# Kernel tuning notes

Measured on AMD Instinct MI355X. Metric: run time of the kernel, lower is better.

Reference implementation:

```python
import jax, jax.numpy as jnp
import numpy as np

B, G, GS = 1024, 2000, 25   # batch, num gene groups, group size
H1, H2, C = 1024, 512, 10
EPS = 1e-5


def _xavier(key, shape, fan_in, fan_out):
    lim = np.sqrt(6.0 / (fan_in + fan_out))
    return jax.random.uniform(key, shape, jnp.float32, -lim, lim)


def setup_inputs() -> dict:
    key = jax.random.key(0)
    ks = jax.random.split(key, 8)
    x = jax.random.normal(ks[0], (B, G * GS), jnp.float32)
    # per-group Linear(GS, 1) weights stacked -> block-diagonal grouped GEMM
    gene_w = _xavier(ks[1], (G, GS), GS, 1)
    gene_b = jnp.zeros((G,), jnp.float32)
    W1 = _xavier(ks[2], (G, H1), G, H1)
    b1 = jnp.zeros((H1,), jnp.float32)
    W2 = _xavier(ks[3], (H1, H2), H1, H2)
    b2 = jnp.zeros((H2,), jnp.float32)
    Wout = _xavier(ks[4], (H2, C), H2, C)
    bout = jnp.zeros((C,), jnp.float32)
    Wres = _xavier(ks[5], (G, C), G, C)
    bres = jnp.zeros((C,), jnp.float32)
    gamma1 = jnp.ones((H1,), jnp.float32); beta1 = jnp.zeros((H1,), jnp.float32)
    gamma2 = jnp.ones((H2,), jnp.float32); beta2 = jnp.zeros((H2,), jnp.float32)
    return dict(x=x, gene_w=gene_w, gene_b=gene_b, W1=W1, b1=b1,
                gamma1=gamma1, beta1=beta1, W2=W2, b2=b2,
                gamma2=gamma2, beta2=beta2, Wout=Wout, bout=bout,
                Wres=Wres, bres=bres)


def _batch_norm(h, gamma, beta):
    # training-mode BatchNorm1d: biased batch statistics over axis 0
    mu = jnp.mean(h, axis=0)
    var = jnp.mean(jnp.square(h - mu), axis=0)
    return gamma * (h - mu) * jax.lax.rsqrt(var + EPS) + beta


def reference(x, gene_w, gene_b, W1, b1, gamma1, beta1, W2, b2,
              gamma2, beta2, Wout, bout, Wres, bres):
    # fused replacement for the per-group Linear(GS,1)+ReLU loop + cat
    xg = x.reshape(B, G, GS)
    g = jax.nn.relu(jnp.einsum('bgk,gk->bg', xg, gene_w) + gene_b)  # [B, G]
    h1 = jax.nn.relu(_batch_norm(g @ W1 + b1, gamma1, beta1))       # [B, H1]
    h2 = jax.nn.relu(_batch_norm(h1 @ W2 + b2, gamma2, beta2))      # [B, H2]
    x_main = h2 @ Wout + bout                                       # [B, C]
    x_res = g @ Wres + bres                                         # [B, C]
    return jax.nn.softmax(x_main + x_res, axis=1)
```

## Files before the change

### kernel.cpp

```cpp
#include <hip/hip_runtime.h>
#include <math.h>

#define NB   1024
#define NG   2000
#define NGS  25
#define KP   2048
#define NH1  1024
#define NH2  512
#define NC   10
#define EPSV 1e-5f
#define GPB  200

typedef __attribute__((ext_vector_type(8))) __bf16 bf16x8;
typedef __attribute__((ext_vector_type(4))) float f32x4;
typedef __attribute__((ext_vector_type(8))) unsigned short u16x8;
typedef __attribute__((ext_vector_type(4))) unsigned short u16x4;

__device__ __forceinline__ unsigned short f2bf(float f) {
  union { float f; unsigned u; } v; v.f = f;
  return (unsigned short)((v.u + 0x7fffu + ((v.u >> 16) & 1u)) >> 16);
}
__device__ __forceinline__ float bf2f(unsigned short b) {
  union { unsigned u; float f; } v; v.u = ((unsigned)b) << 16;
  return v.f;
}

__global__ __launch_bounds__(256) void prep_kernel(
    const float* __restrict__ x, const float* __restrict__ gw,
    const float* __restrict__ gb, unsigned short* __restrict__ g_bf,
    const float* __restrict__ W1, unsigned short* __restrict__ W1bT,
    const float* __restrict__ W2, unsigned short* __restrict__ W2bT,
    float* __restrict__ stats) {
  __shared__ char smem[GPB * NGS * 4];
  int t = threadIdx.x;

  if (blockIdx.y < 10) {
    float* xs = (float*)smem;
    int b = blockIdx.x;
    int blk = blockIdx.y;
    const float4* src = (const float4*)(x + (size_t)b * (NG * NGS) + blk * (GPB * NGS));
    float4* dst = (float4*)xs;
    for (int i = t; i < (GPB * NGS) / 4; i += 256) dst[i] = src[i];
    __syncthreads();
    if (t < GPB) {
      int gi = blk * GPB + t;
      const float* wp = gw + gi * NGS;
      const float* xp = xs + t * NGS;
      float acc = 0.f;
#pragma unroll
      for (int k = 0; k < NGS; ++k) acc = fmaf(xp[k], wp[k], acc);
      acc += gb[gi];
      g_bf[(size_t)b * KP + gi] = f2bf(fmaxf(acc, 0.f));
    } else if (blk == 9 && t < GPB + (KP - NG)) {
      g_bf[(size_t)b * KP + NG + (t - GPB)] = 0;
    }
    return;
  }

  int bx = blockIdx.x;
  if (bx == 640) {
    for (int i = t; i < 3072; i += 256) stats[i] = 0.f;
    return;
  }
  const float* src; unsigned short* dst; int K, N, Kpad, k0, n0;
  if (bx < 512)      { src = W1; dst = W1bT; K = NG;  N = NH1; Kpad = KP;
                       k0 = (bx & 31) * 64; n0 = (bx >> 5) * 64; }
  else if (bx < 640) { int xi = bx - 512;
                       src = W2; dst = W2bT; K = NH1; N = NH2; Kpad = NH1;
                       k0 = (xi & 15) * 64; n0 = (xi >> 4) * 64; }
  else return;

  unsigned short (*ts)[72] = (unsigned short (*)[72])smem;
  int c4 = (t & 15) * 4;
  int r  = t >> 4;
  for (int rr = r; rr < 64; rr += 16) {
    int k = k0 + rr;
    float4 v = make_float4(0.f, 0.f, 0.f, 0.f);
    if (k < K) v = *(const float4*)&src[(size_t)k * N + n0 + c4];
    ts[rr][c4 + 0] = f2bf(v.x); ts[rr][c4 + 1] = f2bf(v.y);
    ts[rr][c4 + 2] = f2bf(v.z); ts[rr][c4 + 3] = f2bf(v.w);
  }
  __syncthreads();
  int rr8 = (t & 7) * 8;
  int cc  = t >> 3;
  for (int c = cc; c < 64; c += 32) {
    u16x8 val;
#pragma unroll
    for (int i = 0; i < 8; ++i) val[i] = ts[rr8 + i][c];
    *(u16x8*)&dst[(size_t)(n0 + c) * Kpad + k0 + rr8] = val;
  }
}

__global__ __launch_bounds__(256) void gemm1_kernel(
    const unsigned short* __restrict__ A,
    const unsigned short* __restrict__ Bt,
    float* __restrict__ C, float* __restrict__ sum, float* __restrict__ sq,
    int M, int N, int Kp) {
  __shared__ unsigned short As[32][72];
  __shared__ unsigned short Bs[64][72];
  int t = threadIdx.x;
  int m0 = blockIdx.y * 32, n0 = blockIdx.x * 64;
  int wave = t >> 6, lane = t & 63;
  int wm = (wave >> 1) * 16, wn = (wave & 1) * 32;
  int fm = lane & 15, fk = (lane >> 4) * 8;
  int srow = t >> 3, skc = (t & 7) * 8;

  f32x4 acc[2];
  acc[0] = (f32x4){0.f, 0.f, 0.f, 0.f};
  acc[1] = (f32x4){0.f, 0.f, 0.f, 0.f};

  const unsigned short* Ap = A + (size_t)(m0 + srow) * Kp + skc;
  const unsigned short* Bp = Bt + (size_t)(n0 + srow) * Kp + skc;
  size_t rstep = 32 * (size_t)Kp;

  u16x8 pa0 = *(const u16x8*)(Ap);
  u16x8 pb0 = *(const u16x8*)(Bp);
  u16x8 pb1 = *(const u16x8*)(Bp + rstep);

  for (int k0 = 0; k0 < Kp; k0 += 64) {
    *(u16x8*)&As[srow][skc]      = pa0;
    *(u16x8*)&Bs[srow][skc]      = pb0;
    *(u16x8*)&Bs[srow + 32][skc] = pb1;
    __syncthreads();
    if (k0 + 64 < Kp) {
      pa0 = *(const u16x8*)(Ap + k0 + 64);
      pb0 = *(const u16x8*)(Bp + k0 + 64);
      pb1 = *(const u16x8*)(Bp + k0 + 64 + rstep);
    }
#pragma unroll
    for (int s = 0; s < 2; ++s) {
      bf16x8 af = *(const bf16x8*)&As[wm + fm][s * 32 + fk];
      bf16x8 b0 = *(const bf16x8*)&Bs[wn + fm][s * 32 + fk];
      bf16x8 b1 = *(const bf16x8*)&Bs[wn + 16 + fm][s * 32 + fk];
      acc[0] = __builtin_amdgcn_mfma_f32_16x16x32_bf16(af, b0, acc[0], 0, 0, 0);
      acc[1] = __builtin_amdgcn_mfma_f32_16x16x32_bf16(af, b1, acc[1], 0, 0, 0);
    }
    __syncthreads();
  }

  int crow = (lane >> 4) * 4, ccol = lane & 15;
#pragma unroll
  for (int j = 0; j < 2; ++j) {
    float s = 0.f, ss = 0.f;
#pragma unroll
    for (int r = 0; r < 4; ++r) {
      float v = acc[j][r];
      int m = m0 + wm + crow + r;
      int n = n0 + wn + j * 16 + ccol;
      C[(size_t)m * N + n] = v;
      s += v;
      ss = fmaf(v, v, ss);
    }
    s  += __shfl_down(s, 32, 64);  s  += __shfl_down(s, 16, 64);
    ss += __shfl_down(ss, 32, 64); ss += __shfl_down(ss, 16, 64);
    if (lane < 16) {
      atomicAdd(&sum[n0 + wn + j * 16 + lane], s);
      atomicAdd(&sq[n0 + wn + j * 16 + lane], ss);
    }
  }
}

__global__ __launch_bounds__(256) void gemm2_kernel(
    const float* __restrict__ A,
    const unsigned short* __restrict__ Bt,
    float* __restrict__ C, const float* __restrict__ sum1,
    const float* __restrict__ sq1, const float* __restrict__ gam1,
    const float* __restrict__ bet1, float* __restrict__ sum2,
    float* __restrict__ sq2, int M, int N, int Kp) {
  __shared__ unsigned short As[32][72];
  __shared__ unsigned short Bs[32][72];
  int t = threadIdx.x;
  int m0 = blockIdx.y * 32, n0 = blockIdx.x * 32;
  int wave = t >> 6, lane = t & 63;
  int wm = (wave >> 1) * 16, wn = (wave & 1) * 16;
  int fm = lane & 15, fk = (lane >> 4) * 8;
  int srow = t >> 3, skc = (t & 7) * 8;

  f32x4 acc = (f32x4){0.f, 0.f, 0.f, 0.f};

  const float* Ap = A + (size_t)(m0 + srow) * Kp + skc;
  const unsigned short* Bp = Bt + (size_t)(n0 + srow) * Kp + skc;

  f32x4 pa0 = *(const f32x4*)(Ap);
  f32x4 pa1 = *(const f32x4*)(Ap + 4);
  u16x8 pb0 = *(const u16x8*)(Bp);

  for (int k0 = 0; k0 < Kp; k0 += 64) {
    float sc[8], sh[8];
#pragma unroll
    for (int i = 0; i < 8; ++i) {
      int k = k0 + skc + i;
      float mu  = sum1[k] * (1.f / NB);
      float var = sq1[k] * (1.f / NB) - mu * mu;
      float rs  = rsqrtf(var + EPSV);
      sc[i] = gam1[k] * rs;
      sh[i] = fmaf(-mu, sc[i], bet1[k]);
    }
    u16x8 a0;
#pragma unroll
    for (int i = 0; i < 4; ++i) {
      a0[i]     = f2bf(fmaxf(fmaf(pa0[i], sc[i],     sh[i]),     0.f));
      a0[i + 4] = f2bf(fmaxf(fmaf(pa1[i], sc[i + 4], sh[i + 4]), 0.f));
    }
    *(u16x8*)&As[srow][skc] = a0;
    *(u16x8*)&Bs[srow][skc] = pb0;
    __syncthreads();
    if (k0 + 64 < Kp) {
      pa0 = *(const f32x4*)(Ap + k0 + 64);
      pa1 = *(const f32x4*)(Ap + k0 + 64 + 4);
      pb0 = *(const u16x8*)(Bp + k0 + 64);
    }
#pragma unroll
    for (int s = 0; s < 2; ++s) {
      bf16x8 af = *(const bf16x8*)&As[wm + fm][s * 32 + fk];
      bf16x8 bf = *(const bf16x8*)&Bs[wn + fm][s * 32 + fk];
      acc = __builtin_amdgcn_mfma_f32_16x16x32_bf16(af, bf, acc, 0, 0, 0);
    }
    __syncthreads();
  }

  int crow = (lane >> 4) * 4, ccol = lane & 15;
  float s = 0.f, ss = 0.f;
#pragma unroll
  for (int r = 0; r < 4; ++r) {
    float v = acc[r];
    int m = m0 + wm + crow + r;
    int n = n0 + wn + ccol;
    C[(size_t)m * N + n] = v;
    s += v;
    ss = fmaf(v, v, ss);
  }
  s  += __shfl_down(s, 32, 64);  s  += __shfl_down(s, 16, 64);
  ss += __shfl_down(ss, 32, 64); ss += __shfl_down(ss, 16, 64);
  if (lane < 16) {
    atomicAdd(&sum2[n0 + wn + lane], s);
    atomicAdd(&sq2[n0 + wn + lane], ss);
  }
}

__global__ __launch_bounds__(256) void final_kernel(
    const float* __restrict__ t2, const float* __restrict__ sum2,
    const float* __restrict__ sq2, const float* __restrict__ gam2,
    const float* __restrict__ bet2, const unsigned short* __restrict__ g_bf,
    const float* __restrict__ Wout, const float* __restrict__ bout,
    const float* __restrict__ Wres, const float* __restrict__ bres,
    float* __restrict__ out) {
  int b = blockIdx.x;
  int t = threadIdx.x;
  float acc[NC] = {};

  if (t < NH2 / 4) {
    float4 tv = *(const float4*)&t2[(size_t)b * NH2 + t * 4];
    float raw[4] = {tv.x, tv.y, tv.z, tv.w};
    float hr[4];
#pragma unroll
    for (int i = 0; i < 4; ++i) {
      int c = t * 4 + i;
      float mu  = sum2[c] * (1.f / NB);
      float var = sq2[c] * (1.f / NB) - mu * mu;
      float rs  = rsqrtf(var + EPSV);
      float scv = gam2[c] * rs;
      hr[i] = fmaxf(fmaf(raw[i], scv, fmaf(-mu, scv, bet2[c])), 0.f);
    }
    const float4* wp = (const float4*)&Wout[t * 4 * NC];
    float w[40];
#pragma unroll
    for (int q = 0; q < 10; ++q) {
      float4 wv = wp[q];
      w[q * 4] = wv.x; w[q * 4 + 1] = wv.y; w[q * 4 + 2] = wv.z; w[q * 4 + 3] = wv.w;
    }
#pragma unroll
    for (int r = 0; r < 4; ++r)
#pragma unroll
      for (int c = 0; c < NC; ++c) acc[c] = fmaf(hr[r], w[r * NC + c], acc[c]);
  }

  for (int u = t; u < NG / 4; u += 256) {
    u16x4 gv = *(const u16x4*)&g_bf[(size_t)b * KP + u * 4];
    float gr[4] = {bf2f(gv[0]), bf2f(gv[1]), bf2f(gv[2]), bf2f(gv[3])};
    const float4* wp = (const float4*)&Wres[u * 4 * NC];
    float w[40];
#pragma unroll
    for (int q = 0; q < 10; ++q) {
      float4 wv = wp[q];
      w[q * 4] = wv.x; w[q * 4 + 1] = wv.y; w[q * 4 + 2] = wv.z; w[q * 4 + 3] = wv.w;
    }
#pragma unroll
    for (int r = 0; r < 4; ++r)
#pragma unroll
      for (int c = 0; c < NC; ++c) acc[c] = fmaf(gr[r], w[r * NC + c], acc[c]);
  }

  __shared__ float red[4][NC];
  __shared__ float logits[NC];
  int lane = t & 63, wave = t >> 6;
#pragma unroll
  for (int c = 0; c < NC; ++c) {
    float v = acc[c];
    for (int off = 32; off > 0; off >>= 1) v += __shfl_down(v, off, 64);
    if (lane == 0) red[wave][c] = v;
  }
  __syncthreads();
  if (t < NC)
    logits[t] = red[0][t] + red[1][t] + red[2][t] + red[3][t] + bout[t] + bres[t];
  __syncthreads();
  if (t == 0) {
    float mx = logits[0];
#pragma unroll
    for (int c = 1; c < NC; ++c) mx = fmaxf(mx, logits[c]);
    float e[NC], s = 0.f;
#pragma unroll
    for (int c = 0; c < NC; ++c) { e[c] = expf(logits[c] - mx); s += e[c]; }
    float inv = 1.f / s;
#pragma unroll
    for (int c = 0; c < NC; ++c) out[(size_t)b * NC + c] = e[c] * inv;
  }
}

extern "C" void kernel_launch(void* const* d_in, const int* in_sizes, int n_in,
                              void* d_out, int out_size, void* d_ws, size_t ws_size,
                              hipStream_t stream) {
  const float* x      = (const float*)d_in[0];
  const float* gw     = (const float*)d_in[1];
  const float* gb     = (const float*)d_in[2];
  const float* W1     = (const float*)d_in[3];
  const float* gamma1 = (const float*)d_in[5];
  const float* beta1  = (const float*)d_in[6];
  const float* W2     = (const float*)d_in[7];
  const float* gamma2 = (const float*)d_in[9];
  const float* beta2  = (const float*)d_in[10];
  const float* Wout   = (const float*)d_in[11];
  const float* bout   = (const float*)d_in[12];
  const float* Wres   = (const float*)d_in[13];
  const float* bres   = (const float*)d_in[14];
  float* out = (float*)d_out;

  char* p = (char*)d_ws;
  unsigned short* g_bf = (unsigned short*)p; p += (size_t)NB * KP * 2;
  unsigned short* W1bT = (unsigned short*)p; p += (size_t)NH1 * KP * 2;
  unsigned short* W2bT = (unsigned short*)p; p += (size_t)NH2 * NH1 * 2;
  float* t1 = (float*)p; p += (size_t)NB * NH1 * 4;
  float* t2 = (float*)p; p += (size_t)NB * NH2 * 4;
  float* stats = (float*)p;
  float* sum1 = stats, *sq1 = stats + 1024, *sum2 = stats + 2048, *sq2 = stats + 2560;

  prep_kernel<<<dim3(NB, 11), 256, 0, stream>>>(x, gw, gb, g_bf,
                                                W1, W1bT, W2, W2bT, stats);

  gemm1_kernel<<<dim3(NH1 / 64, NB / 32), 256, 0, stream>>>(
      g_bf, W1bT, t1, sum1, sq1, NB, NH1, KP);

  gemm2_kernel<<<dim3(NH2 / 32, NB / 32), 256, 0, stream>>>(
      t1, W2bT, t2, sum1, sq1, gamma1, beta1, sum2, sq2, NB, NH2, NH1);

  final_kernel<<<NB, 256, 0, stream>>>(t2, sum2, sq2, gamma2, beta2, g_bf,
                                       Wout, bout, Wres, bres, out);
}
```

Baseline: 366.2 us.

## Fuse GEMM1, GEMM2 and head into one cooperative kernel with grid syncs

Merges the three post-prep kernels into a single cooperative kernel of 512 blocks that uses grid-wide syncs in place of kernel boundaries. GEMM1 also switches to 32x32x16 MFMA with a 128-wide K tile, splitting K across wave pairs and reducing the two halves through shared memory. The aim is to cut launch gaps and raise MFMA efficiency in GEMM1. In exchange, the cooperative launch needs all 512 blocks resident at once, each stage is limited to 512 blocks, and the final softmax stage now handles two rows per block.

```diff
diff --git a/kernel.cpp b/kernel.cpp
--- a/kernel.cpp
+++ b/kernel.cpp
@@ -1,5 +1,8 @@
 #include <hip/hip_runtime.h>
+#include <hip/hip_cooperative_groups.h>
 #include <math.h>
+
+namespace cg = cooperative_groups;
 
 #define NB   1024
 #define NG   2000
@@ -11,10 +14,11 @@
 #define EPSV 1e-5f
 #define GPB  200
 
-typedef __attribute__((ext_vector_type(8))) __bf16 bf16x8;
-typedef __attribute__((ext_vector_type(4))) float f32x4;
-typedef __attribute__((ext_vector_type(8))) unsigned short u16x8;
-typedef __attribute__((ext_vector_type(4))) unsigned short u16x4;
+typedef __attribute__((ext_vector_type(8)))  __bf16 bf16x8;
+typedef __attribute__((ext_vector_type(4)))  float  f32x4;
+typedef __attribute__((ext_vector_type(16))) float  f32x16;
+typedef __attribute__((ext_vector_type(8)))  unsigned short u16x8;
+typedef __attribute__((ext_vector_type(4)))  unsigned short u16x4;
 
 __device__ __forceinline__ unsigned short f2bf(float f) {
   union { float f; unsigned u; } v; v.f = f;
@@ -91,229 +95,255 @@
   }
 }
 
-__global__ __launch_bounds__(256) void gemm1_kernel(
-    const unsigned short* __restrict__ A,
-    const unsigned short* __restrict__ Bt,
-    float* __restrict__ C, float* __restrict__ sum, float* __restrict__ sq,
-    int M, int N, int Kp) {
-  __shared__ unsigned short As[32][72];
-  __shared__ unsigned short Bs[64][72];
+__global__ __launch_bounds__(256) void fused_kernel(
+    const unsigned short* __restrict__ g_bf,
+    const unsigned short* __restrict__ W1bT,
+    const unsigned short* __restrict__ W2bT,
+    float* __restrict__ t1, float* __restrict__ t2,
+    float* __restrict__ stats,
+    const float* __restrict__ gam1, const float* __restrict__ bet1,
+    const float* __restrict__ gam2, const float* __restrict__ bet2,
+    const float* __restrict__ Wout, const float* __restrict__ bout,
+    const float* __restrict__ Wres, const float* __restrict__ bres,
+    float* __restrict__ out) {
+  __shared__ char smem[26112];
+  __shared__ float red[4][NC];
+  __shared__ float logits[NC];
+  cg::grid_group grid = cg::this_grid();
   int t = threadIdx.x;
-  int m0 = blockIdx.y * 32, n0 = blockIdx.x * 64;
+  int blk = blockIdx.x;
   int wave = t >> 6, lane = t & 63;
-  int wm = (wave >> 1) * 16, wn = (wave & 1) * 32;
-  int fm = lane & 15, fk = (lane >> 4) * 8;
-  int srow = t >> 3, skc = (t & 7) * 8;
-
-  f32x4 acc[2];
-  acc[0] = (f32x4){0.f, 0.f, 0.f, 0.f};
-  acc[1] = (f32x4){0.f, 0.f, 0.f, 0.f};
-
-  const unsigned short* Ap = A + (size_t)(m0 + srow) * Kp + skc;
-  const unsigned short* Bp = Bt + (size_t)(n0 + srow) * Kp + skc;
-  size_t rstep = 32 * (size_t)Kp;
-
-  u16x8 pa0 = *(const u16x8*)(Ap);
-  u16x8 pb0 = *(const u16x8*)(Bp);
-  u16x8 pb1 = *(const u16x8*)(Bp + rstep);
-
-  for (int k0 = 0; k0 < Kp; k0 += 64) {
-    *(u16x8*)&As[srow][skc]      = pa0;
-    *(u16x8*)&Bs[srow][skc]      = pb0;
-    *(u16x8*)&Bs[srow + 32][skc] = pb1;
+
+  {
+    unsigned short (*As)[136] = (unsigned short (*)[136])smem;
+    unsigned short (*Bs)[136] = (unsigned short (*)[136])(smem + 8704);
+    int m0 = (blk >> 4) * 32;
+    int n0 = (blk & 15) * 64;
+    int h = wave & 1;
+    int p = wave >> 1;
+    int l31 = lane & 31, l5 = lane >> 5;
+
+    int ar = t >> 3, ac = (t & 7) * 16;
+    int br = t >> 2, bc = (t & 3) * 32;
+    const unsigned short* Ap = g_bf + (size_t)(m0 + ar) * KP + ac;
+    const unsigned short* Bp = W1bT + (size_t)(n0 + br) * KP + bc;
+
+    f32x16 acc;
+#pragma unroll
+    for (int q = 0; q < 16; ++q) acc[q] = 0.f;
+
+    u16x8 pa0 = *(const u16x8*)(Ap);
+    u16x8 pa1 = *(const u16x8*)(Ap + 8);
+    u16x8 pb0 = *(const u16x8*)(Bp);
+    u16x8 pb1 = *(const u16x8*)(Bp + 8);
+    u16x8 pb2 = *(const u16x8*)(Bp + 16);
+    u16x8 pb3 = *(const u16x8*)(Bp + 24);
+
+    for (int k0 = 0; k0 < KP; k0 += 128) {
+      *(u16x8*)&As[ar][ac]      = pa0;
+      *(u16x8*)&As[ar][ac + 8]  = pa1;
+      *(u16x8*)&Bs[br][bc]      = pb0;
+      *(u16x8*)&Bs[br][bc + 8]  = pb1;
+      *(u16x8*)&Bs[br][bc + 16] = pb2;
+      *(u16x8*)&Bs[br][bc + 24] = pb3;
+      __syncthreads();
+      if (k0 + 128 < KP) {
+        pa0 = *(const u16x8*)(Ap + k0 + 128);
+        pa1 = *(const u16x8*)(Ap + k0 + 136);
+        pb0 = *(const u16x8*)(Bp + k0 + 128);
+        pb1 = *(const u16x8*)(Bp + k0 + 136);
+        pb2 = *(const u16x8*)(Bp + k0 + 144);
+        pb3 = *(const u16x8*)(Bp + k0 + 152);
+      }
+      int cb = p * 64 + l5 * 8;
+#pragma unroll
+      for (int s = 0; s < 4; ++s) {
+        bf16x8 av = *(const bf16x8*)&As[l31][cb + s * 16];
+        bf16x8 bv = *(const bf16x8*)&Bs[h * 32 + l31][cb + s * 16];
+        acc = __builtin_amdgcn_mfma_f32_32x32x16_bf16(av, bv, acc, 0, 0, 0);
+      }
+      __syncthreads();
+    }
+    float* ebuf = (float*)(smem + 8704);
+    if (p == 1) {
+      float* dst = ebuf + (size_t)(h * 64 + lane) * 16;
+#pragma unroll
+      for (int q = 0; q < 4; ++q) {
+        f32x4 v = {acc[q * 4], acc[q * 4 + 1], acc[q * 4 + 2], acc[q * 4 + 3]};
+        *(f32x4*)(dst + q * 4) = v;
+      }
+    }
     __syncthreads();
-    if (k0 + 64 < Kp) {
-      pa0 = *(const u16x8*)(Ap + k0 + 64);
-      pb0 = *(const u16x8*)(Bp + k0 + 64);
-      pb1 = *(const u16x8*)(Bp + k0 + 64 + rstep);
-    }
-#pragma unroll
-    for (int s = 0; s < 2; ++s) {
-      bf16x8 af = *(const bf16x8*)&As[wm + fm][s * 32 + fk];
-      bf16x8 b0 = *(const bf16x8*)&Bs[wn + fm][s * 32 + fk];
-      bf16x8 b1 = *(const bf16x8*)&Bs[wn + 16 + fm][s * 32 + fk];
-      acc[0] = __builtin_amdgcn_mfma_f32_16x16x32_bf16(af, b0, acc[0], 0, 0, 0);
-      acc[1] = __builtin_amdgcn_mfma_f32_16x16x32_bf16(af, b1, acc[1], 0, 0, 0);
-    }
-    __syncthreads();
-  }
-
-  int crow = (lane >> 4) * 4, ccol = lane & 15;
-#pragma unroll
-  for (int j = 0; j < 2; ++j) {
+    if (p == 0) {
+      const float* src = ebuf + (size_t)(h * 64 + lane) * 16;
+      float s = 0.f, ss = 0.f;
+#pragma unroll
+      for (int r = 0; r < 16; ++r) {
+        float v = acc[r] + src[r];
+        int row = m0 + (r & 3) + 8 * (r >> 2) + 4 * l5;
+        t1[(size_t)row * NH1 + n0 + h * 32 + l31] = v;
+        s += v;
+        ss = fmaf(v, v, ss);
+      }
+      s  += __shfl_down(s, 32, 64);
+      ss += __shfl_down(ss, 32, 64);
+      if (lane < 32) {
+        atomicAdd(&stats[n0 + h * 32 + lane], s);
+        atomicAdd(&stats[1024 + n0 + h * 32 + lane], ss);
+      }
+    }
+  }
+
+  grid.sync();
+
+  {
+    unsigned short (*As)[72] = (unsigned short (*)[72])smem;
+    unsigned short (*Bs)[72] = (unsigned short (*)[72])(smem + 4608);
+    const float* sum1 = stats;
+    const float* sq1  = stats + 1024;
+    float* sum2 = stats + 2048;
+    float* sq2  = stats + 2560;
+    int m0 = (blk >> 4) * 32, n0 = (blk & 15) * 32;
+    int wm = (wave >> 1) * 16, wn = (wave & 1) * 16;
+    int fm = lane & 15, fk = (lane >> 4) * 8;
+    int srow = t >> 3, skc = (t & 7) * 8;
+
+    f32x4 acc = {0.f, 0.f, 0.f, 0.f};
+
+    const float* Ap = t1 + (size_t)(m0 + srow) * NH1 + skc;
+    const unsigned short* Bp = W2bT + (size_t)(n0 + srow) * NH1 + skc;
+
+    f32x4 pa0 = *(const f32x4*)(Ap);
+    f32x4 pa1 = *(const f32x4*)(Ap + 4);
+    u16x8 pb0 = *(const u16x8*)(Bp);
+
+    for (int k0 = 0; k0 < NH1; k0 += 64) {
+      float sc[8], sh[8];
+#pragma unroll
+      for (int i = 0; i < 8; ++i) {
+        int k = k0 + skc + i;
+        float mu  = sum1[k] * (1.f / NB);
+        float var = sq1[k] * (1.f / NB) - mu * mu;
+        float rs  = rsqrtf(var + EPSV);
+        sc[i] = gam1[k] * rs;
+        sh[i] = fmaf(-mu, sc[i], bet1[k]);
+      }
+      u16x8 a0;
+#pragma unroll
+      for (int i = 0; i < 4; ++i) {
+        a0[i]     = f2bf(fmaxf(fmaf(pa0[i], sc[i],     sh[i]),     0.f));
+        a0[i + 4] = f2bf(fmaxf(fmaf(pa1[i], sc[i + 4], sh[i + 4]), 0.f));
+      }
+      *(u16x8*)&As[srow][skc] = a0;
+      *(u16x8*)&Bs[srow][skc] = pb0;
+      __syncthreads();
+      if (k0 + 64 < NH1) {
+        pa0 = *(const f32x4*)(Ap + k0 + 64);
+        pa1 = *(const f32x4*)(Ap + k0 + 64 + 4);
+        pb0 = *(const u16x8*)(Bp + k0 + 64);
+      }
+#pragma unroll
+      for (int s = 0; s < 2; ++s) {
+        bf16x8 af = *(const bf16x8*)&As[wm + fm][s * 32 + fk];
+        bf16x8 bf = *(const bf16x8*)&Bs[wn + fm][s * 32 + fk];
+        acc = __builtin_amdgcn_mfma_f32_16x16x32_bf16(af, bf, acc, 0, 0, 0);
+      }
+      __syncthreads();
+    }
+
+    int crow = (lane >> 4) * 4, ccol = lane & 15;
     float s = 0.f, ss = 0.f;
 #pragma unroll
     for (int r = 0; r < 4; ++r) {
-      float v = acc[j][r];
+      float v = acc[r];
       int m = m0 + wm + crow + r;
-      int n = n0 + wn + j * 16 + ccol;
-      C[(size_t)m * N + n] = v;
+      int n = n0 + wn + ccol;
+      t2[(size_t)m * NH2 + n] = v;
       s += v;
       ss = fmaf(v, v, ss);
     }
     s  += __shfl_down(s, 32, 64);  s  += __shfl_down(s, 16, 64);
     ss += __shfl_down(ss, 32, 64); ss += __shfl_down(ss, 16, 64);
     if (lane < 16) {
-      atomicAdd(&sum[n0 + wn + j * 16 + lane], s);
-      atomicAdd(&sq[n0 + wn + j * 16 + lane], ss);
-    }
-  }
-}
-
-__global__ __launch_bounds__(256) void gemm2_kernel(
-    const float* __restrict__ A,
-    const unsigned short* __restrict__ Bt,
-    float* __restrict__ C, const float* __restrict__ sum1,
-    const float* __restrict__ sq1, const float* __restrict__ gam1,
-    const float* __restrict__ bet1, float* __restrict__ sum2,
-    float* __restrict__ sq2, int M, int N, int Kp) {
-  __shared__ unsigned short As[32][72];
-  __shared__ unsigned short Bs[32][72];
-  int t = threadIdx.x;
-  int m0 = blockIdx.y * 32, n0 = blockIdx.x * 32;
-  int wave = t >> 6, lane = t & 63;
-  int wm = (wave >> 1) * 16, wn = (wave & 1) * 16;
-  int fm = lane & 15, fk = (lane >> 4) * 8;
-  int srow = t >> 3, skc = (t & 7) * 8;
-
-  f32x4 acc = (f32x4){0.f, 0.f, 0.f, 0.f};
-
-  const float* Ap = A + (size_t)(m0 + srow) * Kp + skc;
-  const unsigned short* Bp = Bt + (size_t)(n0 + srow) * Kp + skc;
-
-  f32x4 pa0 = *(const f32x4*)(Ap);
-  f32x4 pa1 = *(const f32x4*)(Ap + 4);
-  u16x8 pb0 = *(const u16x8*)(Bp);
-
-  for (int k0 = 0; k0 < Kp; k0 += 64) {
-    float sc[8], sh[8];
-#pragma unroll
-    for (int i = 0; i < 8; ++i) {
-      int k = k0 + skc + i;
-      float mu  = sum1[k] * (1.f / NB);
-      float var = sq1[k] * (1.f / NB) - mu * mu;
-      float rs  = rsqrtf(var + EPSV);
-      sc[i] = gam1[k] * rs;
-      sh[i] = fmaf(-mu, sc[i], bet1[k]);
-    }
-    u16x8 a0;
-#pragma unroll
-    for (int i = 0; i < 4; ++i) {
-      a0[i]     = f2bf(fmaxf(fmaf(pa0[i], sc[i],     sh[i]),     0.f));
-      a0[i + 4] = f2bf(fmaxf(fmaf(pa1[i], sc[i + 4], sh[i + 4]), 0.f));
-    }
-    *(u16x8*)&As[srow][skc] = a0;
-    *(u16x8*)&Bs[srow][skc] = pb0;
-    __syncthreads();
-    if (k0 + 64 < Kp) {
-      pa0 = *(const f32x4*)(Ap + k0 + 64);
-      pa1 = *(const f32x4*)(Ap + k0 + 64 + 4);
-      pb0 = *(const u16x8*)(Bp + k0 + 64);
-    }
-#pragma unroll
-    for (int s = 0; s < 2; ++s) {
-      bf16x8 af = *(const bf16x8*)&As[wm + fm][s * 32 + fk];
-      bf16x8 bf = *(const bf16x8*)&Bs[wn + fm][s * 32 + fk];
-      acc = __builtin_amdgcn_mfma_f32_16x16x32_bf16(af, bf, acc, 0, 0, 0);
-    }
-    __syncthreads();
-  }
-
-  int crow = (lane >> 4) * 4, ccol = lane & 15;
-  float s = 0.f, ss = 0.f;
-#pragma unroll
-  for (int r = 0; r < 4; ++r) {
-    float v = acc[r];
-    int m = m0 + wm + crow + r;
-    int n = n0 + wn + ccol;
-    C[(size_t)m * N + n] = v;
-    s += v;
-    ss = fmaf(v, v, ss);
-  }
-  s  += __shfl_down(s, 32, 64);  s  += __shfl_down(s, 16, 64);
-  ss += __shfl_down(ss, 32, 64); ss += __shfl_down(ss, 16, 64);
-  if (lane < 16) {
-    atomicAdd(&sum2[n0 + wn + lane], s);
-    atomicAdd(&sq2[n0 + wn + lane], ss);
-  }
-}
-
-__global__ __launch_bounds__(256) void final_kernel(
-    const float* __restrict__ t2, const float* __restrict__ sum2,
-    const float* __restrict__ sq2, const float* __restrict__ gam2,
-    const float* __restrict__ bet2, const unsigned short* __restrict__ g_bf,
-    const float* __restrict__ Wout, const float* __restrict__ bout,
-    const float* __restrict__ Wres, const float* __restrict__ bres,
-    float* __restrict__ out) {
-  int b = blockIdx.x;
-  int t = threadIdx.x;
-  float acc[NC] = {};
-
-  if (t < NH2 / 4) {
-    float4 tv = *(const float4*)&t2[(size_t)b * NH2 + t * 4];
-    float raw[4] = {tv.x, tv.y, tv.z, tv.w};
-    float hr[4];
-#pragma unroll
-    for (int i = 0; i < 4; ++i) {
-      int c = t * 4 + i;
-      float mu  = sum2[c] * (1.f / NB);
-      float var = sq2[c] * (1.f / NB) - mu * mu;
-      float rs  = rsqrtf(var + EPSV);
-      float scv = gam2[c] * rs;
-      hr[i] = fmaxf(fmaf(raw[i], scv, fmaf(-mu, scv, bet2[c])), 0.f);
-    }
-    const float4* wp = (const float4*)&Wout[t * 4 * NC];
-    float w[40];
-#pragma unroll
-    for (int q = 0; q < 10; ++q) {
-      float4 wv = wp[q];
-      w[q * 4] = wv.x; w[q * 4 + 1] = wv.y; w[q * 4 + 2] = wv.z; w[q * 4 + 3] = wv.w;
-    }
-#pragma unroll
-    for (int r = 0; r < 4; ++r)
-#pragma unroll
-      for (int c = 0; c < NC; ++c) acc[c] = fmaf(hr[r], w[r * NC + c], acc[c]);
-  }
-
-  for (int u = t; u < NG / 4; u += 256) {
-    u16x4 gv = *(const u16x4*)&g_bf[(size_t)b * KP + u * 4];
-    float gr[4] = {bf2f(gv[0]), bf2f(gv[1]), bf2f(gv[2]), bf2f(gv[3])};
-    const float4* wp = (const float4*)&Wres[u * 4 * NC];
-    float w[40];
-#pragma unroll
-    for (int q = 0; q < 10; ++q) {
-      float4 wv = wp[q];
-      w[q * 4] = wv.x; w[q * 4 + 1] = wv.y; w[q * 4 + 2] = wv.z; w[q * 4 + 3] = wv.w;
-    }
-#pragma unroll
-    for (int r = 0; r < 4; ++r)
-#pragma unroll
-      for (int c = 0; c < NC; ++c) acc[c] = fmaf(gr[r], w[r * NC + c], acc[c]);
-  }
-
-  __shared__ float red[4][NC];
-  __shared__ float logits[NC];
-  int lane = t & 63, wave = t >> 6;
-#pragma unroll
-  for (int c = 0; c < NC; ++c) {
-    float v = acc[c];
-    for (int off = 32; off > 0; off >>= 1) v += __shfl_down(v, off, 64);
-    if (lane == 0) red[wave][c] = v;
-  }
-  __syncthreads();
-  if (t < NC)
-    logits[t] = red[0][t] + red[1][t] + red[2][t] + red[3][t] + bout[t] + bres[t];
-  __syncthreads();
-  if (t == 0) {
-    float mx = logits[0];
-#pragma unroll
-    for (int c = 1; c < NC; ++c) mx = fmaxf(mx, logits[c]);
-    float e[NC], s = 0.f;
-#pragma unroll
-    for (int c = 0; c < NC; ++c) { e[c] = expf(logits[c] - mx); s += e[c]; }
-    float inv = 1.f / s;
-#pragma unroll
-    for (int c = 0; c < NC; ++c) out[(size_t)b * NC + c] = e[c] * inv;
+      atomicAdd(&sum2[n0 + wn + lane], s);
+      atomicAdd(&sq2[n0 + wn + lane], ss);
+    }
+  }
+
+  grid.sync();
+
+  {
+    const float* sum2 = stats + 2048;
+    const float* sq2  = stats + 2560;
+    for (int rr = 0; rr < 2; ++rr) {
+      int b = blk * 2 + rr;
+      __syncthreads();
+      float acc[NC] = {};
+
+      if (t < NH2 / 4) {
+        float4 tv = *(const float4*)&t2[(size_t)b * NH2 + t * 4];
+        float raw[4] = {tv.x, tv.y, tv.z, tv.w};
+        float hr[4];
+#pragma unroll
+        for (int i = 0; i < 4; ++i) {
+          int c = t * 4 + i;
+          float mu  = sum2[c] * (1.f / NB);
+          float var = sq2[c] * (1.f / NB) - mu * mu;
+          float rs  = rsqrtf(var + EPSV);
+          float scv = gam2[c] * rs;
+          hr[i] = fmaxf(fmaf(raw[i], scv, fmaf(-mu, scv, bet2[c])), 0.f);
+        }
+        const float4* wp = (const float4*)&Wout[t * 4 * NC];
+        float w[40];
+#pragma unroll
+        for (int q = 0; q < 10; ++q) {
+          float4 wv = wp[q];
+          w[q * 4] = wv.x; w[q * 4 + 1] = wv.y; w[q * 4 + 2] = wv.z; w[q * 4 + 3] = wv.w;
+        }
+#pragma unroll
+        for (int r = 0; r < 4; ++r)
+#pragma unroll
+          for (int c = 0; c < NC; ++c) acc[c] = fmaf(hr[r], w[r * NC + c], acc[c]);
+      }
+
+      for (int u = t; u < NG / 4; u += 256) {
+        u16x4 gv = *(const u16x4*)&g_bf[(size_t)b * KP + u * 4];
+        float gr[4] = {bf2f(gv[0]), bf2f(gv[1]), bf2f(gv[2]), bf2f(gv[3])};
+        const float4* wp = (const float4*)&Wres[u * 4 * NC];
+        float w[40];
+#pragma unroll
+        for (int q = 0; q < 10; ++q) {
+          float4 wv = wp[q];
+          w[q * 4] = wv.x; w[q * 4 + 1] = wv.y; w[q * 4 + 2] = wv.z; w[q * 4 + 3] = wv.w;
+        }
+#pragma unroll
+        for (int r = 0; r < 4; ++r)
+#pragma unroll
+          for (int c = 0; c < NC; ++c) acc[c] = fmaf(gr[r], w[r * NC + c], acc[c]);
+      }
+
+#pragma unroll
+      for (int c = 0; c < NC; ++c) {
+        float v = acc[c];
+        for (int off = 32; off > 0; off >>= 1) v += __shfl_down(v, off, 64);
+        if (lane == 0) red[wave][c] = v;
+      }
+      __syncthreads();
+      if (t < NC)
+        logits[t] = red[0][t] + red[1][t] + red[2][t] + red[3][t] + bout[t] + bres[t];
+      __syncthreads();
+      if (t == 0) {
+        float mx = logits[0];
+#pragma unroll
+        for (int c = 1; c < NC; ++c) mx = fmaxf(mx, logits[c]);
+        float e[NC], sm = 0.f;
+#pragma unroll
+        for (int c = 0; c < NC; ++c) { e[c] = expf(logits[c] - mx); sm += e[c]; }
+        float inv = 1.f / sm;
+#pragma unroll
+        for (int c = 0; c < NC; ++c) out[(size_t)b * NC + c] = e[c] * inv;
+      }
+    }
   }
 }
 
@@ -342,17 +372,13 @@
   float* t1 = (float*)p; p += (size_t)NB * NH1 * 4;
   float* t2 = (float*)p; p += (size_t)NB * NH2 * 4;
   float* stats = (float*)p;
-  float* sum1 = stats, *sq1 = stats + 1024, *sum2 = stats + 2048, *sq2 = stats + 2560;
 
   prep_kernel<<<dim3(NB, 11), 256, 0, stream>>>(x, gw, gb, g_bf,
                                                 W1, W1bT, W2, W2bT, stats);
 
-  gemm1_kernel<<<dim3(NH1 / 64, NB / 32), 256, 0, stream>>>(
-      g_bf, W1bT, t1, sum1, sq1, NB, NH1, KP);
-
-  gemm2_kernel<<<dim3(NH2 / 32, NB / 32), 256, 0, stream>>>(
-      t1, W2bT, t2, sum1, sq1, gamma1, beta1, sum2, sq2, NB, NH2, NH1);
-
-  final_kernel<<<NB, 256, 0, stream>>>(t2, sum2, sq2, gamma2, beta2, g_bf,
-                                       Wout, bout, Wres, bres, out);
-}
+  void* args[] = {&g_bf, &W1bT, &W2bT, &t1, &t2, &stats,
+                  (void*)&gamma1, (void*)&beta1, (void*)&gamma2, (void*)&beta2,
+                  (void*)&Wout, (void*)&bout, (void*)&Wres, (void*)&bres, &out};
+  hipLaunchCooperativeKernel((void*)fused_kernel, dim3(512), dim3(256),
+                             args, 0, stream);
+}
```

Result: slower. 484.9 us (+32.4%).

## Use 32x32x16 MFMA with split-K across waves in gemm1

Applied to the files above, without the earlier changes.

Replaces gemm1's 16x16x32 MFMA tiling with a 32x32x16 MFMA per wave. Two waves split the K dimension of each 64-wide K tile, and their partial accumulators are reduced through a shared-memory buffer before the epilogue. The LDS row padding also changes from 72 to 68. The goal is fewer MFMA and LDS fragment loads per output, at the cost of an extra LDS reduction, a sync, and idle waves in the epilogue.

```diff
diff --git a/kernel.cpp b/kernel.cpp
--- a/kernel.cpp
+++ b/kernel.cpp
@@ -11,10 +11,12 @@
 #define EPSV 1e-5f
 #define GPB  200
 
-typedef __attribute__((ext_vector_type(8))) __bf16 bf16x8;
-typedef __attribute__((ext_vector_type(4))) float f32x4;
-typedef __attribute__((ext_vector_type(8))) unsigned short u16x8;
-typedef __attribute__((ext_vector_type(4))) unsigned short u16x4;
+
+typedef __attribute__((ext_vector_type(8)))  __bf16 bf16x8;
+typedef __attribute__((ext_vector_type(4)))  float  f32x4;
+typedef __attribute__((ext_vector_type(16))) float  f32x16;
+typedef __attribute__((ext_vector_type(8)))  unsigned short u16x8;
+typedef __attribute__((ext_vector_type(4)))  unsigned short u16x4;
 
 __device__ __forceinline__ unsigned short f2bf(float f) {
   union { float f; unsigned u; } v; v.f = f;
@@ -96,18 +98,20 @@
     const unsigned short* __restrict__ Bt,
     float* __restrict__ C, float* __restrict__ sum, float* __restrict__ sq,
     int M, int N, int Kp) {
-  __shared__ unsigned short As[32][72];
-  __shared__ unsigned short Bs[64][72];
+  __shared__ unsigned short As[32][68];
+  __shared__ unsigned short Bs[64][68];
+  __shared__ float ebuf[2 * 64 * 17];
   int t = threadIdx.x;
   int m0 = blockIdx.y * 32, n0 = blockIdx.x * 64;
   int wave = t >> 6, lane = t & 63;
-  int wm = (wave >> 1) * 16, wn = (wave & 1) * 32;
-  int fm = lane & 15, fk = (lane >> 4) * 8;
+  int h = wave & 1;
+  int p = wave >> 1;
+  int l31 = lane & 31, l5 = lane >> 5;
   int srow = t >> 3, skc = (t & 7) * 8;
 
-  f32x4 acc[2];
-  acc[0] = (f32x4){0.f, 0.f, 0.f, 0.f};
-  acc[1] = (f32x4){0.f, 0.f, 0.f, 0.f};
+  f32x16 acc;
+#pragma unroll
+  for (int q = 0; q < 16; ++q) acc[q] = 0.f;
 
   const unsigned short* Ap = A + (size_t)(m0 + srow) * Kp + skc;
   const unsigned short* Bp = Bt + (size_t)(n0 + srow) * Kp + skc;
@@ -127,35 +131,41 @@
       pb0 = *(const u16x8*)(Bp + k0 + 64);
       pb1 = *(const u16x8*)(Bp + k0 + 64 + rstep);
     }
-#pragma unroll
-    for (int s = 0; s < 2; ++s) {
-      bf16x8 af = *(const bf16x8*)&As[wm + fm][s * 32 + fk];
-      bf16x8 b0 = *(const bf16x8*)&Bs[wn + fm][s * 32 + fk];
-      bf16x8 b1 = *(const bf16x8*)&Bs[wn + 16 + fm][s * 32 + fk];
-      acc[0] = __builtin_amdgcn_mfma_f32_16x16x32_bf16(af, b0, acc[0], 0, 0, 0);
-      acc[1] = __builtin_amdgcn_mfma_f32_16x16x32_bf16(af, b1, acc[1], 0, 0, 0);
-    }
-    __syncthreads();
-  }
-
-  int crow = (lane >> 4) * 4, ccol = lane & 15;
-#pragma unroll
-  for (int j = 0; j < 2; ++j) {
+    int kb = p * 32 + l5 * 8;
+    {
+      bf16x8 av = *(const bf16x8*)&As[l31][kb];
+      bf16x8 bv = *(const bf16x8*)&Bs[h * 32 + l31][kb];
+      acc = __builtin_amdgcn_mfma_f32_32x32x16_bf16(av, bv, acc, 0, 0, 0);
+    }
+    {
+      bf16x8 av = *(const bf16x8*)&As[l31][kb + 16];
+      bf16x8 bv = *(const bf16x8*)&Bs[h * 32 + l31][kb + 16];
+      acc = __builtin_amdgcn_mfma_f32_32x32x16_bf16(av, bv, acc, 0, 0, 0);
+    }
+    __syncthreads();
+  }
+
+  float* eb = ebuf + (size_t)(h * 64 + lane) * 17;
+  if (p == 1) {
+#pragma unroll
+    for (int r = 0; r < 16; ++r) eb[r] = acc[r];
+  }
+  __syncthreads();
+  if (p == 0) {
     float s = 0.f, ss = 0.f;
 #pragma unroll
-    for (int r = 0; r < 4; ++r) {
-      float v = acc[j][r];
-      int m = m0 + wm + crow + r;
-      int n = n0 + wn + j * 16 + ccol;
-      C[(size_t)m * N + n] = v;
+    for (int r = 0; r < 16; ++r) {
+      float v = acc[r] + eb[r];
+      int row = m0 + (r & 3) + 8 * (r >> 2) + 4 * l5;
+      C[(size_t)row * N + n0 + h * 32 + l31] = v;
       s += v;
       ss = fmaf(v, v, ss);
     }
-    s  += __shfl_down(s, 32, 64);  s  += __shfl_down(s, 16, 64);
-    ss += __shfl_down(ss, 32, 64); ss += __shfl_down(ss, 16, 64);
-    if (lane < 16) {
-      atomicAdd(&sum[n0 + wn + j * 16 + lane], s);
-      atomicAdd(&sq[n0 + wn + j * 16 + lane], ss);
+    s  += __shfl_down(s, 32, 64);
+    ss += __shfl_down(ss, 32, 64);
+    if (lane < 32) {
+      atomicAdd(&sum[n0 + h * 32 + lane], s);
+      atomicAdd(&sq[n0 + h * 32 + lane], ss);
     }
   }
 }
```

Measured after the change: 363.4 us. No clear change (-0.8%).
